# Kernel optimization log

Measured on AMD Instinct MI355X. Metric: run time of the kernel, lower is better.

## Reference

```python
import jax, jax.numpy as jnp
import numpy as np

B, S, D = 4, 2048, 1024
H = 16
DH = D // H  # dim_q = dim_k = 64
F = 4096
EPS = 1e-5


def setup_inputs() -> dict:
    key = jax.random.key(0)
    ks = jax.random.split(key, 16)
    sd = 0.02
    inp = {
        'x': jax.random.normal(ks[0], (B, S, D), jnp.float32),
        'wq': jax.random.normal(ks[1], (H, D, DH), jnp.float32) * sd,
        'bq': jnp.zeros((H, DH), jnp.float32),
        'wk': jax.random.normal(ks[2], (H, D, DH), jnp.float32) * sd,
        'bk': jnp.zeros((H, DH), jnp.float32),
        'wv': jax.random.normal(ks[3], (H, D, DH), jnp.float32) * sd,
        'bv': jnp.zeros((H, DH), jnp.float32),
        'wo': jax.random.normal(ks[4], (H * DH, D), jnp.float32) * sd,
        'bo': jnp.zeros((D,), jnp.float32),
        'ln1_g': jnp.ones((D,), jnp.float32),
        'ln1_b': jnp.zeros((D,), jnp.float32),
        'w1': jax.random.normal(ks[5], (D, F), jnp.float32) * sd,
        'b1': jnp.zeros((F,), jnp.float32),
        'w2': jax.random.normal(ks[6], (F, D), jnp.float32) * sd,
        'b2': jnp.zeros((D,), jnp.float32),
        'ln2_g': jnp.ones((D,), jnp.float32),
        'ln2_b': jnp.zeros((D,), jnp.float32),
    }
    return inp


def _layernorm(x, g, b):
    mu = jnp.mean(x, axis=-1, keepdims=True)
    var = jnp.mean(jnp.square(x - mu), axis=-1, keepdims=True)
    return (x - mu) * jax.lax.rsqrt(var + EPS) * g + b


def _encoder_layer(x, wq, bq, wk, bk, wv, bv, wo, bo, ln1_g, ln1_b,
                   w1, b1, w2, b2, ln2_g, ln2_b):
    # Multi-head attention (all heads batched via einsum)
    q = jnp.einsum('bsd,hde->bhse', x, wq) + bq[:, None, :]
    k = jnp.einsum('bsd,hde->bhse', x, wk) + bk[:, None, :]
    v = jnp.einsum('bsd,hde->bhse', x, wv) + bv[:, None, :]
    scores = jnp.einsum('bhqe,bhke->bhqk', q, k) / jnp.sqrt(jnp.float32(DH))
    p = jax.nn.softmax(scores, axis=-1)
    o = jnp.einsum('bhqk,bhke->bhqe', p, v)  # [B,H,S,DH]
    o = o.transpose(0, 2, 1, 3).reshape(B, S, H * DH)  # concat heads
    attn = o @ wo + bo
    y = _layernorm(x + attn, ln1_g, ln1_b)  # post-norm residual
    # Feed-forward
    ff = jax.nn.relu(y @ w1 + b1) @ w2 + b2
    return _layernorm(y + ff, ln2_g, ln2_b)


def reference(x, wq, bq, wk, bk, wv, bv, wo, bo, ln1_g, ln1_b,
              w1, b1, w2, b2, ln2_g, ln2_b):
    return _encoder_layer(x, wq, bq, wk, bk, wv, bv, wo, bo, ln1_g, ln1_b,
                          w1, b1, w2, b2, ln2_g, ln2_b)
```

## Files before the change

### kernel.cpp

```cpp
#include <hip/hip_runtime.h>
#include <stdint.h>


typedef short bf16x8 __attribute__((ext_vector_type(8)));
typedef unsigned short u16x8 __attribute__((ext_vector_type(8)));
typedef float f32x4 __attribute__((ext_vector_type(4)));
typedef unsigned int u32x2 __attribute__((ext_vector_type(2)));

#define MFMA16(a, b, c) __builtin_amdgcn_mfma_f32_16x16x32_bf16((a), (b), (c), 0, 0, 0)

#define QSCALE 0.1803368801111204f

__device__ __forceinline__ float b2f(unsigned short u) {
    union { unsigned u32; float f; } x;
    x.u32 = ((unsigned)u) << 16;
    return x.f;
}
__device__ __forceinline__ unsigned short f2b(float f) {
    union { float f; unsigned u; } x;
    x.f = f;
    unsigned r = x.u + 0x7fff + ((x.u >> 16) & 1);
    return (unsigned short)(r >> 16);
}

__device__ __forceinline__ void gl16(const unsigned short* g, unsigned short* l) {
    __builtin_amdgcn_global_load_lds(
        (__attribute__((address_space(1))) unsigned int*)(unsigned long)g,
        (__attribute__((address_space(3))) unsigned int*)l, 16, 0, 0);
}

__global__ __launch_bounds__(256) void f2b_bulk(const float* __restrict__ in,
                                                unsigned short* __restrict__ out) {
    const long i = ((long)blockIdx.x * 256 + threadIdx.x) * 8;
    float4 a = *(const float4*)&in[i];
    float4 b = *(const float4*)&in[i + 4];
    u16x8 u;
    u[0] = f2b(a.x); u[1] = f2b(a.y); u[2] = f2b(a.z); u[3] = f2b(a.w);
    u[4] = f2b(b.x); u[5] = f2b(b.y); u[6] = f2b(b.z); u[7] = f2b(b.w);
    *(u16x8*)&out[i] = u;
}

__global__ void transpose_f2b(const float* __restrict__ in,
                              unsigned short* __restrict__ out,
                              int R, int C, long in_batch_stride,
                              int out_row0, int out_ld) {
    __shared__ float tile[32][33];
    const int batch = blockIdx.z;
    const float* src = in + (long)batch * in_batch_stride;
    const int c0 = blockIdx.x * 32, r0 = blockIdx.y * 32;
    const int tx = threadIdx.x, ty = threadIdx.y;
#pragma unroll
    for (int i = 0; i < 32; i += 8)
        tile[ty + i][tx] = src[(long)(r0 + ty + i) * C + c0 + tx];
    __syncthreads();
#pragma unroll
    for (int i = 0; i < 32; i += 8)
        out[(long)(out_row0 + batch * C + c0 + ty + i) * out_ld + r0 + tx] =
            f2b(tile[tx][ty + i]);
}

__global__ void transpose_v(const unsigned short* __restrict__ qkv,
                            unsigned short* __restrict__ vt) {
    __shared__ unsigned short tile[32][33];
    const int bh = blockIdx.z;
    const int b = bh >> 4, h = bh & 15;
    const int s0 = blockIdx.x * 32, e0 = blockIdx.y * 32;
    const int tx = threadIdx.x, ty = threadIdx.y;
    const unsigned short* src = qkv + ((long)b * 2048) * 3072 + 2048 + h * 64;
#pragma unroll
    for (int i = 0; i < 32; i += 8)
        tile[ty + i][tx] = src[(long)(s0 + ty + i) * 3072 + e0 + tx];
    __syncthreads();
    unsigned short* dst = vt + ((long)bh * 64) * 2048;
#pragma unroll
    for (int i = 0; i < 32; i += 8)
        dst[(long)(e0 + ty + i) * 2048 + s0 + tx] = tile[tx][ty + i];
}

__global__ void concat_bias(const float* __restrict__ bq,
                            const float* __restrict__ bk,
                            const float* __restrict__ bv,
                            float* __restrict__ out) {
    int n = blockIdx.x * 256 + threadIdx.x;
    out[n] = (n < 1024) ? bq[n] : (n < 2048) ? bk[n - 1024] : bv[n - 2048];
}

__device__ __forceinline__ float to_f(float v) { return v; }
__device__ __forceinline__ float to_f(unsigned short v) { return b2f(v); }

template <typename RT>
__global__ __launch_bounds__(512, 2) void gemm256(
    const unsigned short* __restrict__ A, const unsigned short* __restrict__ Bt,
    unsigned short* __restrict__ C, const float* __restrict__ bias,
    const RT* __restrict__ resid, int M, int N, int K, int op) {
    __shared__ __align__(16) unsigned short As[4][256 * 32];
    __shared__ __align__(16) unsigned short Bs[4][256 * 32];
    const int tid = threadIdx.x;
    const int lane = tid & 63;
    const int wave = tid >> 6;
    const int quad = lane >> 4, lr = lane & 15;
    const int wr = wave >> 2, wc = wave & 3;

    const int nx = gridDim.x;
    const int nwg = nx * gridDim.y;
    const int orig = blockIdx.y * nx + blockIdx.x;
    const int wg = (orig & 7) * (nwg >> 3) + (orig >> 3);
    const long n0 = (long)(wg % nx) * 256;
    const long m0 = (long)(wg / nx) * 256;

    f32x4 acc[8][4] = {};

    const int trow = tid >> 2;
    const int tch = ((tid & 3) ^ ((tid >> 3) & 3)) * 8;
    const unsigned short* gA0 = A + (m0 + trow) * (long)K + tch;
    const unsigned short* gA1 = A + (m0 + 128 + trow) * (long)K + tch;
    const unsigned short* gB0 = Bt + (n0 + trow) * (long)K + tch;
    const unsigned short* gB1 = Bt + (n0 + 128 + trow) * (long)K + tch;
    unsigned short* const dA = &As[0][0] + tid * 8;
    unsigned short* const dB = &Bs[0][0] + tid * 8;

    int aoff[8], boff[4];
#pragma unroll
    for (int mi = 0; mi < 8; mi++) {
        const int r = wr * 128 + mi * 16 + lr;
        aoff[mi] = r * 32 + (quad ^ ((r >> 1) & 3)) * 8;
    }
#pragma unroll
    for (int ni = 0; ni < 4; ni++) {
        const int r = wc * 64 + ni * 16 + lr;
        boff[ni] = r * 32 + (quad ^ ((r >> 1) & 3)) * 8;
    }

#define STAGE_A(si)                                                   \
    {                                                                 \
        gl16(gA0 + (long)(si) * 32, dA + ((si) & 3) * 8192);          \
        gl16(gA1 + (long)(si) * 32, dA + ((si) & 3) * 8192 + 4096);   \
    }
#define STAGE_B(si)                                                   \
    {                                                                 \
        gl16(gB0 + (long)(si) * 32, dB + ((si) & 3) * 8192);          \
        gl16(gB1 + (long)(si) * 32, dB + ((si) & 3) * 8192 + 4096);   \
    }

    const int S = K >> 5;
    for (int s = 0; s < 3; s++) {
        STAGE_A(s);
        STAGE_B(s);
    }
    asm volatile("s_waitcnt vmcnt(8)" ::: "memory");
    __builtin_amdgcn_s_barrier();

    for (int s = 0; s < S; ++s) {
        const int slot = s & 3;
        const unsigned short* as_ = &As[slot][0];
        const unsigned short* bs_ = &Bs[slot][0];
        const bool st = (s + 3) < S;
        bf16x8 af[8], bf[4];
#pragma unroll
        for (int mi = 0; mi < 8; mi++) af[mi] = *(const bf16x8*)&as_[aoff[mi]];
        bf[0] = *(const bf16x8*)&bs_[boff[0]];
        bf[1] = *(const bf16x8*)&bs_[boff[1]];
        if (st) STAGE_A(s + 3);
        __builtin_amdgcn_s_barrier();
        asm volatile("s_waitcnt lgkmcnt(0)" ::: "memory");
        __builtin_amdgcn_sched_barrier(0);
        __builtin_amdgcn_s_setprio(1);
#pragma unroll
        for (int mi = 0; mi < 8; mi++) {
            acc[mi][0] = MFMA16(af[mi], bf[0], acc[mi][0]);
            acc[mi][1] = MFMA16(af[mi], bf[1], acc[mi][1]);
        }
        __builtin_amdgcn_s_setprio(0);
        __builtin_amdgcn_s_barrier();
        __builtin_amdgcn_sched_barrier(0);
        bf[2] = *(const bf16x8*)&bs_[boff[2]];
        bf[3] = *(const bf16x8*)&bs_[boff[3]];
        if (st) STAGE_B(s + 3);
        __builtin_amdgcn_s_barrier();
        asm volatile("s_waitcnt lgkmcnt(0)" ::: "memory");
        __builtin_amdgcn_sched_barrier(0);
        __builtin_amdgcn_s_setprio(1);
#pragma unroll
        for (int mi = 0; mi < 8; mi++) {
            acc[mi][2] = MFMA16(af[mi], bf[2], acc[mi][2]);
            acc[mi][3] = MFMA16(af[mi], bf[3], acc[mi][3]);
        }
        __builtin_amdgcn_s_setprio(0);
        if (s + 3 < S) {
            asm volatile("s_waitcnt vmcnt(8)" ::: "memory");
        } else if (s + 2 < S) {
            asm volatile("s_waitcnt vmcnt(4)" ::: "memory");
        } else {
            asm volatile("s_waitcnt vmcnt(0)" ::: "memory");
        }
        __builtin_amdgcn_s_barrier();
        __builtin_amdgcn_sched_barrier(0);
    }
#undef STAGE_A
#undef STAGE_B

#pragma unroll
    for (int ni = 0; ni < 4; ni++) {
        const long col = n0 + wc * 64 + ni * 16 + lr;
        const float bv = bias ? bias[col] : 0.0f;
        const float cscale = (op == 2 && col < 1024) ? QSCALE : 1.0f;
#pragma unroll
        for (int mi = 0; mi < 8; mi++) {
#pragma unroll
            for (int r = 0; r < 4; r++) {
                const long row = m0 + wr * 128 + mi * 16 + quad * 4 + r;
                float v = (acc[mi][ni][r] + bv) * cscale;
                if (resid) v += to_f(resid[row * (long)N + col]);
                if (op == 1) v = fmaxf(v, 0.0f);
                C[row * (long)N + col] = f2b(v);
            }
        }
    }
}

__global__ __launch_bounds__(256, 5) void attn_kernel(
    const unsigned short* __restrict__ qkv, const unsigned short* __restrict__ vt,
    unsigned short* __restrict__ o) {
    __shared__ __align__(16) unsigned short Klds[2][64 * 64];
    __shared__ __align__(16) unsigned short Vlds[2][64 * 64];
    const int l = blockIdx.x;
    const int bh = ((l >> 8) << 3) | (l & 7);
    const int qt = (l >> 3) & 31;
    const int b = bh >> 4, h = bh & 15;
    const int tid = threadIdx.x;
    const int wave = tid >> 6, lane = tid & 63;
    const int quad = lane >> 4, lr = lane & 15;
    const long rowbase = (long)b * 2048;
    const int qb = qt * 64 + wave * 16;

    bf16x8 q0, q1;
    {
        const unsigned short* qrow = qkv + (rowbase + qb + lr) * 3072 + h * 64;
        q0 = *(const bf16x8*)&qrow[quad * 8];
        q1 = *(const bf16x8*)&qrow[32 + quad * 8];
    }

    bf16x8 ones;
#pragma unroll
    for (int i = 0; i < 8; i++) ones[i] = (short)0x3F80;

    const int srow = lane >> 3;
    const int sxc = (lane & 7) ^ srow;
    const unsigned short* kp =
        qkv + (rowbase + wave * 16 + srow) * 3072 + 1024 + h * 64 + sxc * 8;
    const unsigned short* vp =
        vt + ((long)bh * 64 + wave * 16 + srow) * 2048 + sxc * 8;
    const long KADV = 64L * 3072;
    unsigned short* const kd0 = &Klds[0][wave * 16 * 64];
    unsigned short* const vd0 = &Vlds[0][wave * 16 * 64];

#define STAGE(bf)                                                     \
    {                                                                 \
        gl16(kp, kd0 + (bf)*4096);                                    \
        gl16(kp + 8 * 3072, kd0 + (bf)*4096 + 8 * 64);                \
        gl16(vp, vd0 + (bf)*4096);                                    \
        gl16(vp + 8 * 2048, vd0 + (bf)*4096 + 8 * 64);                \
    }

    f32x4 oacc[4] = {};
    f32x4 dacc = {};

    const int x7 = lr & 7;
    const int c00 = (quad ^ x7) * 8;
    const int c01 = ((4 | quad) ^ x7) * 8;

    STAGE(0);
    __syncthreads();

    for (int kt = 0; kt < 32; kt++) {
        const int buf = kt & 1;
        if (kt < 31) {
            kp += KADV;
            vp += 64;
            STAGE(buf ^ 1);
        }
        const unsigned short* kb = &Klds[buf][0];
        f32x4 s4[4];
#pragma unroll
        for (int nt = 0; nt < 4; nt++) {
            const unsigned short* krow = kb + (nt * 16 + lr) * 64;
            bf16x8 k0 = *(const bf16x8*)&krow[c00];
            bf16x8 k1 = *(const bf16x8*)&krow[c01];
            f32x4 z = {};
            z = MFMA16(k0, q0, z);
            z = MFMA16(k1, q1, z);
            s4[nt] = z;
        }
        unsigned pwv[4][2];
#pragma unroll
        for (int nt = 0; nt < 4; nt++) {
            float p0 = exp2f(s4[nt][0]);
            float p1 = exp2f(s4[nt][1]);
            float p2 = exp2f(s4[nt][2]);
            float p3 = exp2f(s4[nt][3]);
            asm("v_cvt_pk_bf16_f32 %0, %1, %2"
                : "=v"(pwv[nt][0]) : "v"(p0), "v"(p1));
            asm("v_cvt_pk_bf16_f32 %0, %1, %2"
                : "=v"(pwv[nt][1]) : "v"(p2), "v"(p3));
        }
        unsigned pq[2][4];
#pragma unroll
        for (int kc = 0; kc < 2; kc++)
#pragma unroll
            for (int tl = 0; tl < 2; tl++) {
                u32x2 y = __builtin_amdgcn_permlane32_swap(
                    pwv[2 * kc][tl], pwv[2 * kc + 1][tl], false, false);
                u32x2 z = __builtin_amdgcn_permlane16_swap(y[0], y[1], false, false);
                pq[kc][tl] = z[0];
                pq[kc][2 + tl] = z[1];
            }

        const unsigned short* vb = &Vlds[buf][0];
#pragma unroll
        for (int kc = 0; kc < 2; kc++) {
            union { unsigned u[4]; bf16x8 h; } pu;
            pu.u[0] = pq[kc][0]; pu.u[1] = pq[kc][1];
            pu.u[2] = pq[kc][2]; pu.u[3] = pq[kc][3];
            const int vc = kc ? c01 : c00;
            dacc = MFMA16(ones, pu.h, dacc);
#pragma unroll
            for (int nt = 0; nt < 4; nt++) {
                bf16x8 va = *(const bf16x8*)&vb[(nt * 16 + lr) * 64 + vc];
                oacc[nt] = MFMA16(va, pu.h, oacc[nt]);
            }
        }
        __syncthreads();
    }

    const float rinv = 1.0f / dacc[0];

    const long orow = rowbase + qb + lr;
#pragma unroll
    for (int nt = 0; nt < 4; nt++) {
        ushort4 ov = {f2b(oacc[nt][0] * rinv), f2b(oacc[nt][1] * rinv),
                      f2b(oacc[nt][2] * rinv), f2b(oacc[nt][3] * rinv)};
        *(ushort4*)&o[orow * 1024 + h * 64 + nt * 16 + quad * 4] = ov;
    }
#undef STAGE
}

__device__ __forceinline__ void st4(float* p, float a, float b, float c, float d) {
    float4 v = {a, b, c, d};
    *(float4*)p = v;
}
__device__ __forceinline__ void st4(unsigned short* p, float a, float b, float c,
                                    float d) {
    ushort4 v = {f2b(a), f2b(b), f2b(c), f2b(d)};
    *(ushort4*)p = v;
}

template <typename OT>
__global__ __launch_bounds__(256) void ln_kernel(
    const unsigned short* __restrict__ in, const float* __restrict__ g,
    const float* __restrict__ b, OT* __restrict__ out) {
    __shared__ float red[4];
    const long row = blockIdx.x;
    const int tid = threadIdx.x;
    ushort4 u = *(const ushort4*)&in[row * 1024 + tid * 4];
    float v[4] = {b2f(u.x), b2f(u.y), b2f(u.z), b2f(u.w)};
    float s = v[0] + v[1] + v[2] + v[3];
#pragma unroll
    for (int off = 32; off > 0; off >>= 1) s += __shfl_down(s, off, 64);
    if ((tid & 63) == 0) red[tid >> 6] = s;
    __syncthreads();
    const float mu = (red[0] + red[1] + red[2] + red[3]) * (1.0f / 1024.0f);
    __syncthreads();
    float d[4], sq = 0.f;
#pragma unroll
    for (int i = 0; i < 4; i++) { d[i] = v[i] - mu; sq += d[i] * d[i]; }
#pragma unroll
    for (int off = 32; off > 0; off >>= 1) sq += __shfl_down(sq, off, 64);
    if ((tid & 63) == 0) red[tid >> 6] = sq;
    __syncthreads();
    const float var = (red[0] + red[1] + red[2] + red[3]) * (1.0f / 1024.0f);
    const float rs = rsqrtf(var + 1e-5f);
    float4 gu = *(const float4*)&g[tid * 4];
    float4 bu = *(const float4*)&b[tid * 4];
    st4(&out[row * 1024 + tid * 4], d[0] * rs * gu.x + bu.x,
        d[1] * rs * gu.y + bu.y, d[2] * rs * gu.z + bu.z,
        d[3] * rs * gu.w + bu.w);
}

extern "C" void kernel_launch(void* const* d_in, const int* in_sizes, int n_in,
                              void* d_out, int out_size, void* d_ws, size_t ws_size,
                              hipStream_t stream) {
    (void)in_sizes; (void)n_in; (void)out_size; (void)ws_size;
    const float* x   = (const float*)d_in[0];
    const float* wq  = (const float*)d_in[1];
    const float* bq  = (const float*)d_in[2];
    const float* wk  = (const float*)d_in[3];
    const float* bk  = (const float*)d_in[4];
    const float* wv  = (const float*)d_in[5];
    const float* bv  = (const float*)d_in[6];
    const float* wo  = (const float*)d_in[7];
    const float* bo  = (const float*)d_in[8];
    const float* g1  = (const float*)d_in[9];
    const float* be1 = (const float*)d_in[10];
    const float* w1  = (const float*)d_in[11];
    const float* b1  = (const float*)d_in[12];
    const float* w2  = (const float*)d_in[13];
    const float* b2  = (const float*)d_in[14];
    const float* g2  = (const float*)d_in[15];
    const float* be2 = (const float*)d_in[16];

    char* ws = (char*)d_ws;
    const size_t MB = 1024 * 1024;
    unsigned short* WT_QKV = (unsigned short*)(ws + 0);
    unsigned short* WT_O   = (unsigned short*)(ws + 6 * MB);
    unsigned short* WT_1   = (unsigned short*)(ws + 8 * MB);
    unsigned short* WT_2   = (unsigned short*)(ws + 16 * MB);
    float*          BQKV   = (float*)(ws + 24 * MB);
    unsigned short* XB     = (unsigned short*)(ws + 25 * MB);
    unsigned short* QKV    = (unsigned short*)(ws + 41 * MB);
    unsigned short* O      = (unsigned short*)(ws + 89 * MB);
    unsigned short* R1     = (unsigned short*)(ws + 25 * MB);
    unsigned short* Y      = (unsigned short*)(ws + 41 * MB);
    unsigned short* R2     = (unsigned short*)(ws + 57 * MB);
    unsigned short* Hb     = (unsigned short*)(ws + 73 * MB);
    unsigned short* VT     = (unsigned short*)(ws + 137 * MB);
    float*          OUT    = (float*)d_out;

    const dim3 tb(32, 8, 1);
    transpose_f2b<<<dim3(2, 32, 16), tb, 0, stream>>>(wq, WT_QKV, 1024, 64, 65536L, 0, 1024);
    transpose_f2b<<<dim3(2, 32, 16), tb, 0, stream>>>(wk, WT_QKV, 1024, 64, 65536L, 1024, 1024);
    transpose_f2b<<<dim3(2, 32, 16), tb, 0, stream>>>(wv, WT_QKV, 1024, 64, 65536L, 2048, 1024);
    transpose_f2b<<<dim3(32, 32, 1), tb, 0, stream>>>(wo, WT_O, 1024, 1024, 0L, 0, 1024);
    transpose_f2b<<<dim3(128, 32, 1), tb, 0, stream>>>(w1, WT_1, 1024, 4096, 0L, 0, 1024);
    transpose_f2b<<<dim3(32, 128, 1), tb, 0, stream>>>(w2, WT_2, 4096, 1024, 0L, 0, 4096);
    concat_bias<<<dim3(12), 256, 0, stream>>>(bq, bk, bv, BQKV);
    f2b_bulk<<<dim3(4096), 256, 0, stream>>>(x, XB);

    gemm256<unsigned short><<<dim3(12, 32), 512, 0, stream>>>(
        XB, WT_QKV, QKV, BQKV, (const unsigned short*)nullptr, 8192, 3072, 1024, 2);
    transpose_v<<<dim3(64, 2, 64), tb, 0, stream>>>(QKV, VT);
    attn_kernel<<<dim3(2048), 256, 0, stream>>>(QKV, VT, O);
    gemm256<float><<<dim3(4, 32), 512, 0, stream>>>(
        O, WT_O, R1, bo, x, 8192, 1024, 1024, 0);
    ln_kernel<unsigned short><<<dim3(8192), 256, 0, stream>>>(R1, g1, be1, Y);
    gemm256<unsigned short><<<dim3(16, 32), 512, 0, stream>>>(
        Y, WT_1, Hb, b1, (const unsigned short*)nullptr, 8192, 4096, 1024, 1);
    gemm256<unsigned short><<<dim3(4, 32), 512, 0, stream>>>(
        Hb, WT_2, R2, b2, Y, 8192, 1024, 4096, 0);
    ln_kernel<float><<<dim3(8192), 256, 0, stream>>>(R2, g2, be2, OUT);
}
```

Measured before the change: 669.0 us.

## Add 256x128-tile triple-buffered GEMM for QKV, out-proj and FFN2

Adds a new GEMM kernel with a 256x128 output tile, K-step 64, a three-slot LDS ring and two half-stage loads interleaved with MFMA phases. It replaces the larger-tile gemm256 for the QKV, output-projection and second FFN GEMMs, doubling the grid so the narrow-N GEMMs fill more CUs. The block-ID remap is kept so L2 reuse of A and B stays similar. The cost is that each tile reuses loaded data less, LDS use per block rises, and the deeper software pipeline adds barriers per K-step.

After: 579.7 us. 1.15x faster.

```diff
diff --git a/kernel.cpp b/kernel.cpp
--- a/kernel.cpp
+++ b/kernel.cpp
@@ -209,6 +209,144 @@
 #pragma unroll
             for (int r = 0; r < 4; r++) {
                 const long row = m0 + wr * 128 + mi * 16 + quad * 4 + r;
+                float v = (acc[mi][ni][r] + bv) * cscale;
+                if (resid) v += to_f(resid[row * (long)N + col]);
+                if (op == 1) v = fmaxf(v, 0.0f);
+                C[row * (long)N + col] = f2b(v);
+            }
+        }
+    }
+}
+
+template <int TAG, typename RT>
+__global__ __launch_bounds__(512, 2) void gemmK64(
+    const unsigned short* __restrict__ A, const unsigned short* __restrict__ Bt,
+    unsigned short* __restrict__ C, const float* __restrict__ bias,
+    const RT* __restrict__ resid, int M, int N, int K, int op) {
+    __shared__ __align__(16) unsigned short As[3][256 * 64];
+    __shared__ __align__(16) unsigned short Bs[3][128 * 64];
+    const int tid = threadIdx.x;
+    const int lane = tid & 63;
+    const int wave = tid >> 6;
+    const int quad = lane >> 4, lr = lane & 15;
+    const int wr = wave >> 1, wc = wave & 1;
+
+    const int nx = gridDim.x;
+    const int nwg = nx * gridDim.y;
+    const int orig = blockIdx.y * nx + blockIdx.x;
+    const int wg = (orig & 7) * (nwg >> 3) + (orig >> 3);
+    const long n0 = (long)(wg % nx) * 128;
+    const long m0 = (long)(wg / nx) * 256;
+
+    f32x4 acc[4][4] = {};
+
+    const int trow = tid >> 3;
+    const int tch = ((tid & 7) ^ ((tid >> 4) & 7)) * 8;
+    const unsigned short* gA = A + (m0 + trow) * (long)K + tch;
+    const unsigned short* gB = Bt + (n0 + trow) * (long)K + tch;
+    const long rs64 = 64 * (long)K;
+    unsigned short* const dA = &As[0][0] + tid * 8;
+    unsigned short* const dB = &Bs[0][0] + tid * 8;
+
+    int aoff[2][4], boff[2][4];
+#pragma unroll
+    for (int kc = 0; kc < 2; kc++) {
+#pragma unroll
+        for (int mi = 0; mi < 4; mi++) {
+            const int r = wr * 64 + mi * 16 + lr;
+            aoff[kc][mi] = r * 64 + (((kc << 2) | quad) ^ ((r >> 1) & 7)) * 8;
+        }
+#pragma unroll
+        for (int ni = 0; ni < 4; ni++) {
+            const int r = wc * 64 + ni * 16 + lr;
+            boff[kc][ni] = r * 64 + (((kc << 2) | quad) ^ ((r >> 1) & 7)) * 8;
+        }
+    }
+
+#define KSTAGE_H1(si)                                                   \
+    {                                                                   \
+        const long _kk = (long)(si) * 64;                               \
+        const int _sl = (si) % 3;                                       \
+        gl16(gA + _kk, dA + _sl * 16384);                               \
+        gl16(gA + rs64 + _kk, dA + _sl * 16384 + 4096);                 \
+        gl16(gB + _kk, dB + _sl * 8192);                                \
+    }
+#define KSTAGE_H2(si)                                                   \
+    {                                                                   \
+        const long _kk = (long)(si) * 64;                               \
+        const int _sl = (si) % 3;                                       \
+        gl16(gA + 2 * rs64 + _kk, dA + _sl * 16384 + 8192);             \
+        gl16(gA + 3 * rs64 + _kk, dA + _sl * 16384 + 12288);            \
+        gl16(gB + rs64 + _kk, dB + _sl * 8192 + 4096);                  \
+    }
+
+    const int S = K >> 6;
+    KSTAGE_H1(0);
+    KSTAGE_H2(0);
+    KSTAGE_H1(1);
+    KSTAGE_H2(1);
+    asm volatile("s_waitcnt vmcnt(6)" ::: "memory");
+    __builtin_amdgcn_s_barrier();
+
+    for (int s = 0; s < S; ++s) {
+        const int sl = s % 3;
+        const unsigned short* as_ = &As[sl][0];
+        const unsigned short* bs_ = &Bs[sl][0];
+        const bool st = (s + 2) < S;
+        bf16x8 a0[4], b0[4], a1[4], b1[4];
+#pragma unroll
+        for (int mi = 0; mi < 4; mi++) a0[mi] = *(const bf16x8*)&as_[aoff[0][mi]];
+#pragma unroll
+        for (int ni = 0; ni < 4; ni++) b0[ni] = *(const bf16x8*)&bs_[boff[0][ni]];
+        if (st) KSTAGE_H1(s + 2);
+        __builtin_amdgcn_s_barrier();
+        asm volatile("s_waitcnt lgkmcnt(0)" ::: "memory");
+        __builtin_amdgcn_sched_barrier(0);
+        __builtin_amdgcn_s_setprio(1);
+#pragma unroll
+        for (int mi = 0; mi < 4; mi++)
+#pragma unroll
+            for (int ni = 0; ni < 4; ni++)
+                acc[mi][ni] = MFMA16(a0[mi], b0[ni], acc[mi][ni]);
+        __builtin_amdgcn_s_setprio(0);
+        __builtin_amdgcn_s_barrier();
+        __builtin_amdgcn_sched_barrier(0);
+#pragma unroll
+        for (int mi = 0; mi < 4; mi++) a1[mi] = *(const bf16x8*)&as_[aoff[1][mi]];
+#pragma unroll
+        for (int ni = 0; ni < 4; ni++) b1[ni] = *(const bf16x8*)&bs_[boff[1][ni]];
+        if (st) KSTAGE_H2(s + 2);
+        __builtin_amdgcn_s_barrier();
+        asm volatile("s_waitcnt lgkmcnt(0)" ::: "memory");
+        __builtin_amdgcn_sched_barrier(0);
+        __builtin_amdgcn_s_setprio(1);
+#pragma unroll
+        for (int mi = 0; mi < 4; mi++)
+#pragma unroll
+            for (int ni = 0; ni < 4; ni++)
+                acc[mi][ni] = MFMA16(a1[mi], b1[ni], acc[mi][ni]);
+        __builtin_amdgcn_s_setprio(0);
+        if (st) {
+            asm volatile("s_waitcnt vmcnt(6)" ::: "memory");
+        } else {
+            asm volatile("s_waitcnt vmcnt(0)" ::: "memory");
+        }
+        __builtin_amdgcn_s_barrier();
+        __builtin_amdgcn_sched_barrier(0);
+    }
+#undef KSTAGE_H1
+#undef KSTAGE_H2
+
+#pragma unroll
+    for (int ni = 0; ni < 4; ni++) {
+        const long col = n0 + wc * 64 + ni * 16 + lr;
+        const float bv = bias ? bias[col] : 0.0f;
+        const float cscale = (op == 2 && col < 1024) ? QSCALE : 1.0f;
+#pragma unroll
+        for (int mi = 0; mi < 4; mi++) {
+#pragma unroll
+            for (int r = 0; r < 4; r++) {
+                const long row = m0 + wr * 64 + mi * 16 + quad * 4 + r;
                 float v = (acc[mi][ni][r] + bv) * cscale;
                 if (resid) v += to_f(resid[row * (long)N + col]);
                 if (op == 1) v = fmaxf(v, 0.0f);
@@ -435,16 +573,16 @@
     concat_bias<<<dim3(12), 256, 0, stream>>>(bq, bk, bv, BQKV);
     f2b_bulk<<<dim3(4096), 256, 0, stream>>>(x, XB);
 
-    gemm256<unsigned short><<<dim3(12, 32), 512, 0, stream>>>(
+    gemmK64<0, unsigned short><<<dim3(24, 32), 512, 0, stream>>>(
         XB, WT_QKV, QKV, BQKV, (const unsigned short*)nullptr, 8192, 3072, 1024, 2);
     transpose_v<<<dim3(64, 2, 64), tb, 0, stream>>>(QKV, VT);
     attn_kernel<<<dim3(2048), 256, 0, stream>>>(QKV, VT, O);
-    gemm256<float><<<dim3(4, 32), 512, 0, stream>>>(
+    gemmK64<1, float><<<dim3(8, 32), 512, 0, stream>>>(
         O, WT_O, R1, bo, x, 8192, 1024, 1024, 0);
     ln_kernel<unsigned short><<<dim3(8192), 256, 0, stream>>>(R1, g1, be1, Y);
     gemm256<unsigned short><<<dim3(16, 32), 512, 0, stream>>>(
         Y, WT_1, Hb, b1, (const unsigned short*)nullptr, 8192, 4096, 1024, 1);
-    gemm256<unsigned short><<<dim3(4, 32), 512, 0, stream>>>(
+    gemmK64<2, unsigned short><<<dim3(8, 32), 512, 0, stream>>>(
         Hb, WT_2, R2, b2, Y, 8192, 1024, 4096, 0);
     ln_kernel<float><<<dim3(8192), 256, 0, stream>>>(R2, g2, be2, OUT);
 }
```
